# Optimization experiments

Measured on AMD Instinct MI355X. Metric: run time of the kernel, lower is better.

Reference implementation:

```python
import jax, jax.numpy as jnp
import numpy as np

EPS = 1e-8

def _squash(t, axis=-1):
    sq = jnp.sum(t * t, axis=axis, keepdims=True)
    return (sq / (1.0 + sq)) * t / jnp.sqrt(sq + EPS)

def setup_inputs() -> dict:
    key = jax.random.key(0)
    k1, k2 = jax.random.split(key)
    B, IC, NC, OD, ID = 128, 2048, 16, 16, 8
    x = jax.random.normal(k1, (B, IC, ID), dtype=jnp.float32)
    W = 0.01 * jax.random.normal(k2, (1, IC, NC, OD, ID), dtype=jnp.float32)
    return {"x": x, "W": W}

def reference(x, W):
    # u_hat[b,i,c,o] = sum_d W[0,i,c,o,d] * x[b,i,d]
    u_hat = jnp.einsum('icod,bid->bico', W[0], x)  # [B, IC, NC, OD]
    B, IC, NC, _ = u_hat.shape
    b_ij = jnp.zeros((B, IC, NC, 1), dtype=u_hat.dtype)
    v_j = None
    for _ in range(3):  # fixed 3 routing iterations
        c_ij = jax.nn.softmax(b_ij, axis=2)                 # [B, IC, NC, 1]
        s_j = jnp.sum(c_ij * u_hat, axis=1, keepdims=True)  # [B, 1, NC, OD]
        v_j = _squash(s_j, axis=-1)                          # [B, 1, NC, OD]
        b_ij = b_ij + jnp.sum(u_hat * v_j, axis=-1, keepdims=True)
    return jnp.squeeze(v_j, axis=1)  # [B, NC, OD]
```

## Files before the change

### kernel.cpp

```cpp
#include <hip/hip_runtime.h>
#include <math.h>

#define IC_   2048
#define NC_   16
#define OD_   16
#define ID_   8
#define B_    128
#define LOG2E_ 1.4426950408889634f

#define P1_BB   8
#define P1_CH   64
#define P1_ICPB (IC_/P1_CH)
#define P2_NCH  16
#define P2_IPB  (IC_/P2_NCH)
#define P2_IPW  (P2_IPB/4)

typedef _Float16 h2 __attribute__((ext_vector_type(2)));
typedef _Float16 h8 __attribute__((ext_vector_type(8)));

__device__ __forceinline__ int origco(int lane, int k) {
  return ((lane & 15) << 4) + (lane >> 4) + 4 * k;
}

template<int CTRL>
__device__ __forceinline__ float dpp_add(float x) {
  const int xi = __builtin_bit_cast(int, x);
  const int yi = __builtin_amdgcn_update_dpp(xi, xi, CTRL, 0xF, 0xF, false);
  return x + __builtin_bit_cast(float, yi);
}
__device__ __forceinline__ float row16_sum(float x) {
  x = dpp_add<0x0B1>(x);
  x = dpp_add<0x04E>(x);
  x = dpp_add<0x141>(x);
  x = dpp_add<0x140>(x);
  return x;
}

__device__ __forceinline__ float dot8h(h8 w, h8 x) {
  const h2 w0 = __builtin_shufflevector(w, w, 0, 1), x0 = __builtin_shufflevector(x, x, 0, 1);
  const h2 w1 = __builtin_shufflevector(w, w, 2, 3), x1 = __builtin_shufflevector(x, x, 2, 3);
  const h2 w2 = __builtin_shufflevector(w, w, 4, 5), x2 = __builtin_shufflevector(x, x, 4, 5);
  const h2 w3 = __builtin_shufflevector(w, w, 6, 7), x3 = __builtin_shufflevector(x, x, 6, 7);
  float s = __builtin_amdgcn_fdot2(w0, x0, 0.f, false);
  s = __builtin_amdgcn_fdot2(w1, x1, s, false);
  s = __builtin_amdgcn_fdot2(w2, x2, s, false);
  s = __builtin_amdgcn_fdot2(w3, x3, s, false);
  return s;
}

__global__ __launch_bounds__(256)
void cvt16(const float* __restrict__ in, _Float16* __restrict__ out, int n8) {
  for (int idx = blockIdx.x * 256 + threadIdx.x; idx < n8; idx += gridDim.x * 256) {
    const float4 a = ((const float4*)in)[2 * idx];
    const float4 b = ((const float4*)in)[2 * idx + 1];
    h8 h;
    h[0] = (_Float16)a.x; h[1] = (_Float16)a.y; h[2] = (_Float16)a.z; h[3] = (_Float16)a.w;
    h[4] = (_Float16)b.x; h[5] = (_Float16)b.y; h[6] = (_Float16)b.z; h[7] = (_Float16)b.w;
    ((h8*)out)[idx] = h;
  }
}

__global__ __launch_bounds__(256)
void cvtW(const float* __restrict__ in, _Float16* __restrict__ out) {
  const int idx = blockIdx.x * 256 + threadIdx.x;
  const int ro  = idx & 255;
  const int i   = idx >> 8;
  const int rp  = (ro >> 4) + ((ro & 3) << 4) + (((ro >> 2) & 3) << 6);
  const float4 a = ((const float4*)in)[2 * idx];
  const float4 b = ((const float4*)in)[2 * idx + 1];
  h8 h;
  h[0] = (_Float16)a.x; h[1] = (_Float16)a.y; h[2] = (_Float16)a.z; h[3] = (_Float16)a.w;
  h[4] = (_Float16)b.x; h[5] = (_Float16)b.y; h[6] = (_Float16)b.z; h[7] = (_Float16)b.w;
  *(h8*)(out + ((size_t)i * 256 + rp) * ID_) = h;
}

__global__ __launch_bounds__(256)
void caps_pass1(const _Float16* __restrict__ xh, const _Float16* __restrict__ Wp,
                unsigned int* __restrict__ u_hat, float* __restrict__ s_part) {
  const int bg = blockIdx.x;
  const int ch = blockIdx.y;
  const int tid = threadIdx.x, wid = tid >> 6, lane = tid & 63;

  float acc[P1_BB][4];
#pragma unroll
  for (int bb = 0; bb < P1_BB; ++bb)
#pragma unroll
    for (int k = 0; k < 4; ++k) acc[bb][k] = 0.f;

  for (int t = 0; t < P1_ICPB / 4; ++t) {
    const int i = ch * P1_ICPB + t * 4 + wid;
    const _Float16* wr = Wp + (size_t)i * 2048 + lane * ID_;
    const h8 w0 = *(const h8*)(wr);
    const h8 w1 = *(const h8*)(wr + 512);
    const h8 w2 = *(const h8*)(wr + 1024);
    const h8 w3 = *(const h8*)(wr + 1536);

#pragma unroll
    for (int bb = 0; bb < P1_BB; ++bb) {
      const int b = bg * P1_BB + bb;
      const h8 xv = *(const h8*)(xh + ((size_t)b * IC_ + i) * ID_);
      const float u0 = dot8h(w0, xv);
      const float u1 = dot8h(w1, xv);
      const float u2 = dot8h(w2, xv);
      const float u3 = dot8h(w3, xv);
      acc[bb][0] += u0; acc[bb][1] += u1; acc[bb][2] += u2; acc[bb][3] += u3;
      h2 p0; p0[0] = (_Float16)u0; p0[1] = (_Float16)u1;
      h2 p1; p1[0] = (_Float16)u2; p1[1] = (_Float16)u3;
      uint2 dw;
      dw.x = __builtin_bit_cast(unsigned int, p0);
      dw.y = __builtin_bit_cast(unsigned int, p1);
      *(uint2*)(u_hat + ((size_t)b * IC_ + i) * 128 + lane * 2) = dw;
    }
  }

  __shared__ float red[4][P1_BB * 256];
#pragma unroll
  for (int bb = 0; bb < P1_BB; ++bb)
#pragma unroll
    for (int k = 0; k < 4; ++k)
      red[wid][bb * 256 + origco(lane, k)] = acc[bb][k];
  __syncthreads();
#pragma unroll
  for (int bb = 0; bb < P1_BB; ++bb) {
    const int idx = bb * 256 + tid;
    const float s = red[0][idx] + red[1][idx] + red[2][idx] + red[3][idx];
    s_part[((size_t)(bg * P1_BB + bb) * P1_CH + ch) * 256 + tid] = s;
  }
}

__global__ __launch_bounds__(256)
void caps_wpass(const unsigned int* __restrict__ u_hat, const float* __restrict__ vs,
                float* __restrict__ s_part) {
  const int b   = blockIdx.x;
  const int ich = blockIdx.y;
  const int tid = threadIdx.x, wid = tid >> 6, lane = tid & 63;

  const float vv0 = vs[b * 256 + origco(lane, 0)];
  const float vv1 = vs[b * 256 + origco(lane, 1)];
  const float vv2 = vs[b * 256 + origco(lane, 2)];
  const float vv3 = vs[b * 256 + origco(lane, 3)];

  float a0 = 0.f, a1 = 0.f, a2 = 0.f, a3 = 0.f;
  const unsigned int* up =
      u_hat + ((size_t)b * IC_ + ich * P2_IPB + wid * P2_IPW) * 128 + lane * 2;

#pragma unroll 4
  for (int t = 0; t < P2_IPW; ++t) {
    const uint2 dw = *(const uint2*)(up + (size_t)t * 128);
    const h2 ha = __builtin_bit_cast(h2, dw.x);
    const h2 hb = __builtin_bit_cast(h2, dw.y);
    const float u0 = (float)ha[0], u1 = (float)ha[1];
    const float u2 = (float)hb[0], u3 = (float)hb[1];

    float p = u0 * vv0;
    p = fmaf(u1, vv1, p);
    p = fmaf(u2, vv2, p);
    p = fmaf(u3, vv3, p);
    p += __shfl_xor(p, 16);
    p += __shfl_xor(p, 32);
    const float e = __builtin_amdgcn_exp2f(p);
    const float Z = row16_sum(e);
    const float w = e * __builtin_amdgcn_rcpf(Z);
    a0 = fmaf(w, u0, a0);
    a1 = fmaf(w, u1, a1);
    a2 = fmaf(w, u2, a2);
    a3 = fmaf(w, u3, a3);
  }

  __shared__ float red[4][256];
  red[wid][origco(lane, 0)] = a0;
  red[wid][origco(lane, 1)] = a1;
  red[wid][origco(lane, 2)] = a2;
  red[wid][origco(lane, 3)] = a3;
  __syncthreads();
  const float s = red[0][tid] + red[1][tid] + red[2][tid] + red[3][tid];
  s_part[((size_t)b * P2_NCH + ich) * 256 + tid] = s;
}

__global__ __launch_bounds__(256)
void caps_reduce(const float* __restrict__ s_part, float* __restrict__ vraw,
                 float* __restrict__ vs_next, float* __restrict__ out,
                 const float* __restrict__ v_prev_raw, float scale, int mode, int nch) {
  const int b = blockIdx.x, t = threadIdx.x;
  float s = 0.f;
  for (int ch = 0; ch < nch; ++ch)
    s += s_part[((size_t)b * nch + ch) * 256 + t];
  s *= scale;
  float sq = s * s;
  sq += __shfl_xor(sq, 1); sq += __shfl_xor(sq, 2);
  sq += __shfl_xor(sq, 4); sq += __shfl_xor(sq, 8);
  const float f = sq / ((1.f + sq) * sqrtf(sq + 1e-8f));
  const float v = s * f;
  if (mode == 0) { vraw[b*256+t] = v; vs_next[b*256+t] = v * LOG2E_; }
  else if (mode == 1) { vs_next[b*256+t] = (v + v_prev_raw[b*256+t]) * LOG2E_; }
  else { out[b*256+t] = v; }
}

__device__ __forceinline__ float4 ld4(const float* p) { return *(const float4*)p; }
__device__ __forceinline__ float dot8f(float4 a0, float4 a1, float4 b0, float4 b1) {
  float s = a0.x * b0.x;
  s = fmaf(a0.y, b0.y, s); s = fmaf(a0.z, b0.z, s); s = fmaf(a0.w, b0.w, s);
  s = fmaf(a1.x, b1.x, s); s = fmaf(a1.y, b1.y, s); s = fmaf(a1.z, b1.z, s);
  s = fmaf(a1.w, b1.w, s);
  return s;
}
template<bool UNIFORM, int CH>
__global__ __launch_bounds__(256)
void caps_pass_f32(const float* __restrict__ x, const float* __restrict__ W,
                   const float* __restrict__ vs, float* __restrict__ s_part) {
  constexpr int ICPB  = IC_ / CH;
  constexpr int TITER = ICPB / 4;
  const int bg = blockIdx.x, ch = blockIdx.y, tid = threadIdx.x;
  const int wid = tid >> 6, lane = tid & 63;
  float4 vr[4];
  if (!UNIFORM) {
#pragma unroll
    for (int bb = 0; bb < 4; ++bb) {
      const float* vp = vs + (size_t)(bg * 4 + bb) * 256 + lane;
      vr[bb] = make_float4(vp[0], vp[64], vp[128], vp[192]);
    }
  }
  float4 acc[4];
#pragma unroll
  for (int bb = 0; bb < 4; ++bb) acc[bb] = make_float4(0.f, 0.f, 0.f, 0.f);
  for (int t = 0; t < TITER; ++t) {
    const int i = ch * ICPB + t * 4 + wid;
    const float* wr = W + (size_t)i * 2048 + lane * 8;
    const float4 wa0 = ld4(wr);        const float4 wa1 = ld4(wr + 4);
    const float4 wb0 = ld4(wr + 512);  const float4 wb1 = ld4(wr + 516);
    const float4 wc0 = ld4(wr + 1024); const float4 wc1 = ld4(wr + 1028);
    const float4 wd0 = ld4(wr + 1536); const float4 wd1 = ld4(wr + 1540);
#pragma unroll
    for (int bb = 0; bb < 4; ++bb) {
      const float* xp = x + ((size_t)(bg * 4 + bb) * IC_ + i) * ID_;
      const float4 x0 = ld4(xp), x1 = ld4(xp + 4);
      const float u0 = dot8f(wa0, wa1, x0, x1);
      const float u1 = dot8f(wb0, wb1, x0, x1);
      const float u2 = dot8f(wc0, wc1, x0, x1);
      const float u3 = dot8f(wd0, wd1, x0, x1);
      if (UNIFORM) {
        acc[bb].x += u0; acc[bb].y += u1; acc[bb].z += u2; acc[bb].w += u3;
      } else {
        const float d0 = row16_sum(u0 * vr[bb].x);
        const float d1 = row16_sum(u1 * vr[bb].y);
        const float d2 = row16_sum(u2 * vr[bb].z);
        const float d3 = row16_sum(u3 * vr[bb].w);
        const float e0 = __builtin_amdgcn_exp2f(d0);
        const float e1 = __builtin_amdgcn_exp2f(d1);
        const float e2 = __builtin_amdgcn_exp2f(d2);
        const float e3 = __builtin_amdgcn_exp2f(d3);
        float Z = (e0 + e1) + (e2 + e3);
        Z += __shfl_xor(Z, 16); Z += __shfl_xor(Z, 32);
        const float rr = __builtin_amdgcn_rcpf(Z);
        acc[bb].x = fmaf(e0 * rr, u0, acc[bb].x);
        acc[bb].y = fmaf(e1 * rr, u1, acc[bb].y);
        acc[bb].z = fmaf(e2 * rr, u2, acc[bb].z);
        acc[bb].w = fmaf(e3 * rr, u3, acc[bb].w);
      }
    }
  }
  __shared__ float red[4][4 * 256];
#pragma unroll
  for (int bb = 0; bb < 4; ++bb) {
    red[wid][bb * 256 + lane]       = acc[bb].x;
    red[wid][bb * 256 + lane + 64]  = acc[bb].y;
    red[wid][bb * 256 + lane + 128] = acc[bb].z;
    red[wid][bb * 256 + lane + 192] = acc[bb].w;
  }
  __syncthreads();
#pragma unroll
  for (int bb = 0; bb < 4; ++bb) {
    const int idx = bb * 256 + tid;
    const float s = red[0][idx] + red[1][idx] + red[2][idx] + red[3][idx];
    s_part[((size_t)(bg * 4 + bb) * CH + ch) * 256 + tid] = s;
  }
}

extern "C" void kernel_launch(void* const* d_in, const int* in_sizes, int n_in,
                              void* d_out, int out_size, void* d_ws, size_t ws_size,
                              hipStream_t stream) {
  (void)in_sizes; (void)n_in; (void)out_size;

  const float* x = (const float*)d_in[0];
  const float* W = (const float*)d_in[1];
  float* out = (float*)d_out;

  const size_t u_dw  = (size_t)B_ * IC_ * 128;
  const size_t sp_f  = (size_t)B_ * P1_CH * 256;
  const size_t v_f   = (size_t)B_ * 256;
  const size_t nW    = (size_t)IC_ * 256 * ID_;
  const size_t nX    = (size_t)B_ * IC_ * ID_;
  const size_t need  = u_dw * 4 + sp_f * 4 + 2 * v_f * 4 + (nW + nX) * 2;

  const dim3 blk(256), gridR(B_);

  if (ws_size >= need) {
    unsigned int* u_hat = (unsigned int*)d_ws;
    float* s_part = (float*)(u_hat + u_dw);
    float* v1raw  = s_part + sp_f;
    float* vsb    = v1raw + v_f;
    _Float16* Wh  = (_Float16*)(vsb + v_f);
    _Float16* xh  = Wh + nW;

    cvtW <<<2048, blk, 0, stream>>>(W, Wh);
    cvt16<<<1024, blk, 0, stream>>>(x, xh, (int)(nX / 8));

    caps_pass1<<<dim3(B_ / P1_BB, P1_CH), blk, 0, stream>>>(xh, Wh, u_hat, s_part);
    caps_reduce<<<gridR, blk, 0, stream>>>(s_part, v1raw, vsb, nullptr, nullptr,
                                           1.f / 16.f, 0, P1_CH);
    caps_wpass<<<dim3(B_, P2_NCH), blk, 0, stream>>>(u_hat, vsb, s_part);
    caps_reduce<<<gridR, blk, 0, stream>>>(s_part, nullptr, vsb, nullptr, v1raw,
                                           1.f, 1, P2_NCH);
    caps_wpass<<<dim3(B_, P2_NCH), blk, 0, stream>>>(u_hat, vsb, s_part);
    caps_reduce<<<gridR, blk, 0, stream>>>(s_part, nullptr, nullptr, out, nullptr,
                                           1.f, 2, P2_NCH);
  } else {
    constexpr int CH = 32;
    float* s_part = (float*)d_ws;
    float* v1raw  = s_part + (size_t)B_ * CH * 256;
    float* vsb    = v1raw + (size_t)B_ * 256;
    const dim3 gridP(B_ / 4, CH);
    caps_pass_f32<true , CH><<<gridP, blk, 0, stream>>>(x, W, nullptr, s_part);
    caps_reduce<<<gridR, blk, 0, stream>>>(s_part, v1raw, vsb, nullptr, nullptr, 1.f/16.f, 0, CH);
    caps_pass_f32<false, CH><<<gridP, blk, 0, stream>>>(x, W, vsb, s_part);
    caps_reduce<<<gridR, blk, 0, stream>>>(s_part, nullptr, vsb, nullptr, v1raw, 1.f, 1, CH);
    caps_pass_f32<false, CH><<<gridP, blk, 0, stream>>>(x, W, vsb, s_part);
    caps_reduce<<<gridR, blk, 0, stream>>>(s_part, nullptr, nullptr, out, nullptr, 1.f, 2, CH);
  }
}
```

Measured before the change: 125.8 us.

## Pair input capsules in u_hat layout, fuse conversion kernels, pad LDS reductions

```diff
diff --git a/kernel.cpp b/kernel.cpp
--- a/kernel.cpp
+++ b/kernel.cpp
@@ -12,8 +12,6 @@
 #define P1_CH   64
 #define P1_ICPB (IC_/P1_CH)
 #define P2_NCH  16
-#define P2_IPB  (IC_/P2_NCH)
-#define P2_IPW  (P2_IPB/4)
 
 typedef _Float16 h2 __attribute__((ext_vector_type(2)));
 typedef _Float16 h8 __attribute__((ext_vector_type(8)));
@@ -48,30 +46,34 @@
   return s;
 }
 
-__global__ __launch_bounds__(256)
-void cvt16(const float* __restrict__ in, _Float16* __restrict__ out, int n8) {
-  for (int idx = blockIdx.x * 256 + threadIdx.x; idx < n8; idx += gridDim.x * 256) {
-    const float4 a = ((const float4*)in)[2 * idx];
-    const float4 b = ((const float4*)in)[2 * idx + 1];
+__device__ __forceinline__ unsigned int packh2(float a, float b) {
+  h2 h; h[0] = (_Float16)a; h[1] = (_Float16)b;
+  return __builtin_bit_cast(unsigned int, h);
+}
+
+__global__ __launch_bounds__(256)
+void cvtWX(const float* __restrict__ W, const float* __restrict__ x,
+           _Float16* __restrict__ Wh, _Float16* __restrict__ xh) {
+  if (blockIdx.x < 2048) {
+    const int idx = blockIdx.x * 256 + threadIdx.x;
+    const int ro  = idx & 255;
+    const int i   = idx >> 8;
+    const int rp  = (ro >> 4) + ((ro & 3) << 4) + (((ro >> 2) & 3) << 6);
+    const float4 a = ((const float4*)W)[2 * idx];
+    const float4 b = ((const float4*)W)[2 * idx + 1];
     h8 h;
     h[0] = (_Float16)a.x; h[1] = (_Float16)a.y; h[2] = (_Float16)a.z; h[3] = (_Float16)a.w;
     h[4] = (_Float16)b.x; h[5] = (_Float16)b.y; h[6] = (_Float16)b.z; h[7] = (_Float16)b.w;
-    ((h8*)out)[idx] = h;
-  }
-}
-
-__global__ __launch_bounds__(256)
-void cvtW(const float* __restrict__ in, _Float16* __restrict__ out) {
-  const int idx = blockIdx.x * 256 + threadIdx.x;
-  const int ro  = idx & 255;
-  const int i   = idx >> 8;
-  const int rp  = (ro >> 4) + ((ro & 3) << 4) + (((ro >> 2) & 3) << 6);
-  const float4 a = ((const float4*)in)[2 * idx];
-  const float4 b = ((const float4*)in)[2 * idx + 1];
-  h8 h;
-  h[0] = (_Float16)a.x; h[1] = (_Float16)a.y; h[2] = (_Float16)a.z; h[3] = (_Float16)a.w;
-  h[4] = (_Float16)b.x; h[5] = (_Float16)b.y; h[6] = (_Float16)b.z; h[7] = (_Float16)b.w;
-  *(h8*)(out + ((size_t)i * 256 + rp) * ID_) = h;
+    *(h8*)(Wh + ((size_t)i * 256 + rp) * ID_) = h;
+  } else {
+    const int idx = (blockIdx.x - 2048) * 256 + threadIdx.x;
+    const float4 a = ((const float4*)x)[2 * idx];
+    const float4 b = ((const float4*)x)[2 * idx + 1];
+    h8 h;
+    h[0] = (_Float16)a.x; h[1] = (_Float16)a.y; h[2] = (_Float16)a.z; h[3] = (_Float16)a.w;
+    h[4] = (_Float16)b.x; h[5] = (_Float16)b.y; h[6] = (_Float16)b.z; h[7] = (_Float16)b.w;
+    ((h8*)xh)[idx] = h;
+  }
 }
 
 __global__ __launch_bounds__(256)
@@ -87,43 +89,60 @@
 #pragma unroll
     for (int k = 0; k < 4; ++k) acc[bb][k] = 0.f;
 
-  for (int t = 0; t < P1_ICPB / 4; ++t) {
-    const int i = ch * P1_ICPB + t * 4 + wid;
-    const _Float16* wr = Wp + (size_t)i * 2048 + lane * ID_;
-    const h8 w0 = *(const h8*)(wr);
-    const h8 w1 = *(const h8*)(wr + 512);
-    const h8 w2 = *(const h8*)(wr + 1024);
-    const h8 w3 = *(const h8*)(wr + 1536);
+  for (int t = 0; t < 4; ++t) {
+    const int ip = ch * P1_ICPB + t * 8 + wid * 2;
+    const _Float16* wr0 = Wp + (size_t)ip * 2048 + lane * ID_;
+    const _Float16* wr1 = wr0 + 2048;
+    const h8 wA0 = *(const h8*)(wr0);
+    const h8 wA1 = *(const h8*)(wr0 + 512);
+    const h8 wA2 = *(const h8*)(wr0 + 1024);
+    const h8 wA3 = *(const h8*)(wr0 + 1536);
+    const h8 wB0 = *(const h8*)(wr1);
+    const h8 wB1 = *(const h8*)(wr1 + 512);
+    const h8 wB2 = *(const h8*)(wr1 + 1024);
+    const h8 wB3 = *(const h8*)(wr1 + 1536);
 
 #pragma unroll
     for (int bb = 0; bb < P1_BB; ++bb) {
       const int b = bg * P1_BB + bb;
-      const h8 xv = *(const h8*)(xh + ((size_t)b * IC_ + i) * ID_);
-      const float u0 = dot8h(w0, xv);
-      const float u1 = dot8h(w1, xv);
-      const float u2 = dot8h(w2, xv);
-      const float u3 = dot8h(w3, xv);
-      acc[bb][0] += u0; acc[bb][1] += u1; acc[bb][2] += u2; acc[bb][3] += u3;
-      h2 p0; p0[0] = (_Float16)u0; p0[1] = (_Float16)u1;
-      h2 p1; p1[0] = (_Float16)u2; p1[1] = (_Float16)u3;
-      uint2 dw;
-      dw.x = __builtin_bit_cast(unsigned int, p0);
-      dw.y = __builtin_bit_cast(unsigned int, p1);
-      *(uint2*)(u_hat + ((size_t)b * IC_ + i) * 128 + lane * 2) = dw;
-    }
-  }
-
-  __shared__ float red[4][P1_BB * 256];
+      const _Float16* xp = xh + ((size_t)b * IC_ + ip) * ID_;
+      const h8 xv0 = *(const h8*)(xp);
+      const h8 xv1 = *(const h8*)(xp + ID_);
+
+      const float u00 = dot8h(wA0, xv0);
+      const float u01 = dot8h(wA1, xv0);
+      const float u02 = dot8h(wA2, xv0);
+      const float u03 = dot8h(wA3, xv0);
+      const float u10 = dot8h(wB0, xv1);
+      const float u11 = dot8h(wB1, xv1);
+      const float u12 = dot8h(wB2, xv1);
+      const float u13 = dot8h(wB3, xv1);
+
+      acc[bb][0] += u00 + u10;
+      acc[bb][1] += u01 + u11;
+      acc[bb][2] += u02 + u12;
+      acc[bb][3] += u03 + u13;
+
+      uint4 q;
+      q.x = packh2(u00, u01);
+      q.y = packh2(u02, u03);
+      q.z = packh2(u10, u11);
+      q.w = packh2(u12, u13);
+      *(uint4*)(u_hat + ((size_t)b * 1024 + (ip >> 1)) * 256 + lane * 4) = q;
+    }
+  }
+
+  __shared__ float red[4][P1_BB][272];
 #pragma unroll
   for (int bb = 0; bb < P1_BB; ++bb)
 #pragma unroll
     for (int k = 0; k < 4; ++k)
-      red[wid][bb * 256 + origco(lane, k)] = acc[bb][k];
+      red[wid][bb][((lane >> 4) + 4 * k) * 17 + (lane & 15)] = acc[bb][k];
   __syncthreads();
 #pragma unroll
   for (int bb = 0; bb < P1_BB; ++bb) {
-    const int idx = bb * 256 + tid;
-    const float s = red[0][idx] + red[1][idx] + red[2][idx] + red[3][idx];
+    const int addr = (tid & 15) * 17 + (tid >> 4);
+    const float s = red[0][bb][addr] + red[1][bb][addr] + red[2][bb][addr] + red[3][bb][addr];
     s_part[((size_t)(bg * P1_BB + bb) * P1_CH + ch) * 256 + tid] = s;
   }
 }
@@ -142,38 +161,60 @@
 
   float a0 = 0.f, a1 = 0.f, a2 = 0.f, a3 = 0.f;
   const unsigned int* up =
-      u_hat + ((size_t)b * IC_ + ich * P2_IPB + wid * P2_IPW) * 128 + lane * 2;
+      u_hat + ((size_t)b * 1024 + ich * 64 + wid * 16) * 256 + lane * 4;
 
 #pragma unroll 4
-  for (int t = 0; t < P2_IPW; ++t) {
-    const uint2 dw = *(const uint2*)(up + (size_t)t * 128);
-    const h2 ha = __builtin_bit_cast(h2, dw.x);
-    const h2 hb = __builtin_bit_cast(h2, dw.y);
-    const float u0 = (float)ha[0], u1 = (float)ha[1];
-    const float u2 = (float)hb[0], u3 = (float)hb[1];
-
-    float p = u0 * vv0;
-    p = fmaf(u1, vv1, p);
-    p = fmaf(u2, vv2, p);
-    p = fmaf(u3, vv3, p);
-    p += __shfl_xor(p, 16);
-    p += __shfl_xor(p, 32);
-    const float e = __builtin_amdgcn_exp2f(p);
-    const float Z = row16_sum(e);
-    const float w = e * __builtin_amdgcn_rcpf(Z);
-    a0 = fmaf(w, u0, a0);
-    a1 = fmaf(w, u1, a1);
-    a2 = fmaf(w, u2, a2);
-    a3 = fmaf(w, u3, a3);
-  }
-
-  __shared__ float red[4][256];
-  red[wid][origco(lane, 0)] = a0;
-  red[wid][origco(lane, 1)] = a1;
-  red[wid][origco(lane, 2)] = a2;
-  red[wid][origco(lane, 3)] = a3;
+  for (int t = 0; t < 16; ++t) {
+    const uint4 q = *(const uint4*)(up + (size_t)t * 256);
+
+    {
+      const h2 ha = __builtin_bit_cast(h2, q.x);
+      const h2 hb = __builtin_bit_cast(h2, q.y);
+      const float u0 = (float)ha[0], u1 = (float)ha[1];
+      const float u2 = (float)hb[0], u3 = (float)hb[1];
+      float p = u0 * vv0;
+      p = fmaf(u1, vv1, p);
+      p = fmaf(u2, vv2, p);
+      p = fmaf(u3, vv3, p);
+      p += __shfl_xor(p, 16);
+      p += __shfl_xor(p, 32);
+      const float e = __builtin_amdgcn_exp2f(p);
+      const float Z = row16_sum(e);
+      const float w = e * __builtin_amdgcn_rcpf(Z);
+      a0 = fmaf(w, u0, a0);
+      a1 = fmaf(w, u1, a1);
+      a2 = fmaf(w, u2, a2);
+      a3 = fmaf(w, u3, a3);
+    }
+    {
+      const h2 ha = __builtin_bit_cast(h2, q.z);
+      const h2 hb = __builtin_bit_cast(h2, q.w);
+      const float u0 = (float)ha[0], u1 = (float)ha[1];
+      const float u2 = (float)hb[0], u3 = (float)hb[1];
+      float p = u0 * vv0;
+      p = fmaf(u1, vv1, p);
+      p = fmaf(u2, vv2, p);
+      p = fmaf(u3, vv3, p);
+      p += __shfl_xor(p, 16);
+      p += __shfl_xor(p, 32);
+      const float e = __builtin_amdgcn_exp2f(p);
+      const float Z = row16_sum(e);
+      const float w = e * __builtin_amdgcn_rcpf(Z);
+      a0 = fmaf(w, u0, a0);
+      a1 = fmaf(w, u1, a1);
+      a2 = fmaf(w, u2, a2);
+      a3 = fmaf(w, u3, a3);
+    }
+  }
+
+  __shared__ float red[4][272];
+  red[wid][((lane >> 4) + 0) * 17 + (lane & 15)]  = a0;
+  red[wid][((lane >> 4) + 4) * 17 + (lane & 15)]  = a1;
+  red[wid][((lane >> 4) + 8) * 17 + (lane & 15)]  = a2;
+  red[wid][((lane >> 4) + 12) * 17 + (lane & 15)] = a3;
   __syncthreads();
-  const float s = red[0][tid] + red[1][tid] + red[2][tid] + red[3][tid];
+  const int addr = (tid & 15) * 17 + (tid >> 4);
+  const float s = red[0][addr] + red[1][addr] + red[2][addr] + red[3][addr];
   s_part[((size_t)b * P2_NCH + ich) * 256 + tid] = s;
 }
 
@@ -285,7 +326,7 @@
   const float* W = (const float*)d_in[1];
   float* out = (float*)d_out;
 
-  const size_t u_dw  = (size_t)B_ * IC_ * 128;
+  const size_t u_dw  = (size_t)B_ * 1024 * 256;
   const size_t sp_f  = (size_t)B_ * P1_CH * 256;
   const size_t v_f   = (size_t)B_ * 256;
   const size_t nW    = (size_t)IC_ * 256 * ID_;
@@ -302,8 +343,7 @@
     _Float16* Wh  = (_Float16*)(vsb + v_f);
     _Float16* xh  = Wh + nW;
 
-    cvtW <<<2048, blk, 0, stream>>>(W, Wh);
-    cvt16<<<1024, blk, 0, stream>>>(x, xh, (int)(nX / 8));
+    cvtWX<<<3072, blk, 0, stream>>>(W, x, Wh, xh);
 
     caps_pass1<<<dim3(B_ / P1_BB, P1_CH), blk, 0, stream>>>(xh, Wh, u_hat, s_part);
     caps_reduce<<<gridR, blk, 0, stream>>>(s_part, v1raw, vsb, nullptr, nullptr,
```

Measured after the change: 126.0 us. No clear change (+0.1%).
